# Optimization experiments

Measured on AMD Instinct MI355X. Metric: run time of the kernel, lower is better.

Reference implementation:

```python
import jax, jax.numpy as jnp
import numpy as np

B, LQ, LK = 8, 2048, 2048
HIST_DIM, COMB_DIM, FUSION_DIM = 1024, 1024, 1024


def _linear_params(key, in_dim, out_dim):
    k1, k2 = jax.random.split(key)
    bound = 1.0 / np.sqrt(in_dim)
    W = jax.random.uniform(k1, (out_dim, in_dim), jnp.float32, -bound, bound)
    b = jax.random.uniform(k2, (out_dim,), jnp.float32, -bound, bound)
    return W, b


def setup_inputs() -> dict:
    key = jax.random.key(0)
    ks = jax.random.split(key, 8)
    hW, hb = _linear_params(ks[0], HIST_DIM, FUSION_DIM)
    cW, cb = _linear_params(ks[1], COMB_DIM, FUSION_DIM)
    qW, qb = _linear_params(ks[2], FUSION_DIM, FUSION_DIM)
    kW, kb = _linear_params(ks[3], FUSION_DIM, FUSION_DIM)
    vW, vb = _linear_params(ks[4], FUSION_DIM, FUSION_DIM)
    oW, ob = _linear_params(ks[5], FUSION_DIM, FUSION_DIM)
    return {
        "history_features": jax.random.normal(ks[6], (B, LQ, HIST_DIM), jnp.float32),
        "combined_features": jax.random.normal(ks[7], (B, LK, COMB_DIM), jnp.float32),
        "hW": hW, "hb": hb, "cW": cW, "cb": cb,
        "qW": qW, "qb": qb, "kW": kW, "kb": kb,
        "vW": vW, "vb": vb, "oW": oW, "ob": ob,
    }


def _lin(x, W, b):
    # torch nn.Linear: y = x @ W.T + b
    return jnp.einsum('bld,fd->blf', x, W) + b


def reference(history_features, combined_features, hW, hb, cW, cb, qW, qb, kW, kb, vW, vb, oW, ob):
    h = _lin(history_features, hW, hb)      # [B, LQ, F]
    c = _lin(combined_features, cW, cb)     # [B, LK, F]
    q = _lin(h, qW, qb)
    k = _lin(c, kW, kb)
    v = _lin(c, vW, vb)
    scale = 1.0 / jnp.sqrt(jnp.float32(FUSION_DIM))
    scores = jnp.einsum('bqf,bkf->bqk', q, k) * scale
    attn = jax.nn.softmax(scores, axis=-1)
    attn_out = jnp.einsum('bqk,bkf->bqf', attn, v)
    return _lin(attn_out + q, oW, ob)
```

## Files before the change

### kernel.cpp

```cpp
#include <hip/hip_runtime.h>
#include <stdint.h>

using bf16x8 = __attribute__((ext_vector_type(8))) short;
using f32x4  = __attribute__((ext_vector_type(4))) float;
using u16x4  = __attribute__((ext_vector_type(4))) unsigned short;
using u16x8  = __attribute__((ext_vector_type(8))) unsigned short;

__device__ __forceinline__ unsigned short f2bf(float f) {
  unsigned u = __builtin_bit_cast(unsigned, f);
  u = (u + 0x7FFFu + ((u >> 16) & 1u)) >> 16;
  return (unsigned short)u;
}
__device__ __forceinline__ float bf2f(unsigned short h) {
  unsigned u = ((unsigned)h) << 16;
  return __builtin_bit_cast(float, u);
}

__global__ __launch_bounds__(256) void cvt_f32_to_bf16(
    const float* __restrict__ in, unsigned short* __restrict__ out, long n8) {
  long i = (long)blockIdx.x * blockDim.x + threadIdx.x;
  const long stride = (long)gridDim.x * blockDim.x;
  for (; i < n8; i += stride) {
    float4 a = ((const float4*)in)[2 * i];
    float4 b = ((const float4*)in)[2 * i + 1];
    u16x8 o = { f2bf(a.x), f2bf(a.y), f2bf(a.z), f2bf(a.w),
                f2bf(b.x), f2bf(b.y), f2bf(b.z), f2bf(b.w) };
    ((u16x8*)out)[i] = o;
  }
}

__global__ __launch_bounds__(256) void transpose_cast(
    const float* __restrict__ in, unsigned short* __restrict__ out, int R, int C) {
  __shared__ unsigned short tile[64][68];
  const int c0 = blockIdx.x * 64, r0 = blockIdx.y * 64;
  const int t = threadIdx.x;
#pragma unroll
  for (int i = 0; i < 4; ++i) {
    int ch = t + i * 256;
    int r = ch >> 4, c4 = (ch & 15) * 4;
    float4 v = *(const float4*)&in[(size_t)(r0 + r) * C + c0 + c4];
    u16x4 o = { f2bf(v.x), f2bf(v.y), f2bf(v.z), f2bf(v.w) };
    *(u16x4*)&tile[r][c4] = o;
  }
  __syncthreads();
#pragma unroll
  for (int i = 0; i < 4; ++i) {
    int ch = t + i * 256;
    int r = ch >> 4, c4 = (ch & 15) * 4;
    u16x4 v;
#pragma unroll
    for (int j = 0; j < 4; ++j) v[j] = tile[c4 + j][r];
    *(u16x4*)&out[(size_t)(c0 + r) * R + r0 + c4] = v;
  }
}

__global__ __launch_bounds__(256) void bias_matvec(
    const float* __restrict__ W, const float* __restrict__ x,
    const float* __restrict__ b, float* __restrict__ out, int n) {
  const int row = blockIdx.x;
  const float* wr = W + (long)row * n;
  float s = 0.f;
  for (int j = threadIdx.x; j < n; j += 256) s += wr[j] * x[j];
#pragma unroll
  for (int o = 32; o; o >>= 1) s += __shfl_xor(s, o);
  __shared__ float red[4];
  if ((threadIdx.x & 63) == 0) red[threadIdx.x >> 6] = s;
  __syncthreads();
  if (threadIdx.x == 0) out[row] = red[0] + red[1] + red[2] + red[3] + b[row];
}

__global__ __launch_bounds__(256) void merge_invl(
    const float* __restrict__ Lpart, float* __restrict__ invL, long nrows) {
  long r = (long)blockIdx.x * 256 + threadIdx.x;
  if (r < nrows) {
    const float* p = Lpart + r * 8;
    float s = 0.f;
#pragma unroll
    for (int i = 0; i < 8; ++i) s += p[i];
    invL[r] = 1.f / s;
  }
}

template <int EPI>
__global__ __launch_bounds__(256, 4) void gemm_bt(
    const unsigned short* __restrict__ A, const unsigned short* __restrict__ B,
    void* __restrict__ C, const float* __restrict__ bias,
    int M, int N, int K, float scale) {
  __shared__ unsigned short lA[2][128][32];
  __shared__ unsigned short lB[2][128][32];
  const int t = threadIdx.x;
  const int gx = gridDim.x, gy = gridDim.y;
  int bid = blockIdx.x + gx * blockIdx.y;
  const int nwg = gx * gy;
  const int chunk = nwg >> 3;
  int lid = (bid & 7) * chunk + (bid >> 3);
  const int bn = lid % gx;
  const int bm = lid / gx;

  const unsigned short* Ab = A + (long)bm * 128 * K;
  const unsigned short* Bb = B + (long)bn * 128 * K;

  const int lane = t & 63;
  const int wv = t >> 6, wm = wv >> 1, wn = wv & 1;
  const int fr = lane & 15, kg = lane >> 4;
  const int srow  = t >> 2;
  const int scol  = (t & 3) * 8;
  const int wbyte = (t >> 6) * 1024;

  f32x4 acc[4][4] = {};
  const int NT = K >> 5;

  auto stage = [&](int buf, int kt) {
    const unsigned short* sa = Ab + kt * 32;
    const unsigned short* sb = Bb + kt * 32;
#pragma unroll
    for (int p = 0; p < 2; ++p) {
      const unsigned short* srcA = sa + (long)(p * 64 + srow) * K + scol;
      const unsigned short* srcB = sb + (long)(p * 64 + srow) * K + scol;
      char* dA = (char*)(&lA[buf][0][0]) + p * 4096 + wbyte;
      char* dB = (char*)(&lB[buf][0][0]) + p * 4096 + wbyte;
      __builtin_amdgcn_global_load_lds(
          (const __attribute__((address_space(1))) void*)srcA,
          (__attribute__((address_space(3))) void*)dA, 16, 0, 0);
      __builtin_amdgcn_global_load_lds(
          (const __attribute__((address_space(1))) void*)srcB,
          (__attribute__((address_space(3))) void*)dB, 16, 0, 0);
    }
  };

  stage(0, 0);
  for (int kt = 0; kt < NT; ++kt) {
    const int cur = kt & 1;
    __syncthreads();
    if (kt + 1 < NT) stage(cur ^ 1, kt + 1);
    bf16x8 av[4], bv[4];
#pragma unroll
    for (int m = 0; m < 4; ++m)
      av[m] = *(const bf16x8*)&lA[cur][wm * 64 + m * 16 + fr][kg * 8];
#pragma unroll
    for (int n = 0; n < 4; ++n)
      bv[n] = *(const bf16x8*)&lB[cur][wn * 64 + n * 16 + fr][kg * 8];
#pragma unroll
    for (int m = 0; m < 4; ++m)
#pragma unroll
      for (int n = 0; n < 4; ++n)
        acc[m][n] = __builtin_amdgcn_mfma_f32_16x16x32_bf16(av[m], bv[n], acc[m][n], 0, 0, 0);
  }

  const int row0 = bm * 128 + wm * 64 + kg * 4;
  const int col0 = bn * 128 + wn * 64 + fr;
#pragma unroll
  for (int m = 0; m < 4; ++m)
#pragma unroll
    for (int n = 0; n < 4; ++n) {
      const int col = col0 + n * 16;
#pragma unroll
      for (int r = 0; r < 4; ++r) {
        const int row = row0 + m * 16 + r;
        float v = acc[m][n][r];
        if constexpr (EPI == 1) v *= scale; else v += bias[col];
        ((unsigned short*)C)[(long)row * N + col] = f2bf(v);
      }
    }
}

template <int EPI>
__global__ __launch_bounds__(512, 2) void gemm256(
    const unsigned short* __restrict__ A, const unsigned short* __restrict__ B,
    void* __restrict__ C, const float* __restrict__ bias,
    const unsigned short* __restrict__ resid, float* __restrict__ aux,
    int N, int K, long sA, long sB, long sC, long sR, float scale) {
  __shared__ char lds[131072];
  const int t = threadIdx.x;
  const int lane = t & 63, wid = t >> 6;

  const int gx = gridDim.x, gy = gridDim.y;
  int bid = blockIdx.x + gx * (blockIdx.y + gy * blockIdx.z);
  const int nwg = gx * gy * (int)gridDim.z;
  const int chunk = nwg >> 3;
  int lid = (bid & 7) * chunk + (bid >> 3);
  const int bn = lid % gx; lid /= gx;
  const int bm = lid % gy;
  const int bz = lid / gy;

  const unsigned short* Ab = A + (long)bz * sA + (long)bm * 256 * K;
  const unsigned short* Bb = B + (long)bz * sB + (long)bn * 256 * K;

  const int colswz = ((lane & 3) * 8) ^ ((lane >> 5) * 16);
  const int r0s = (wid >> 1) * 16 + (lane >> 2);
  const int scol = (wid & 1) * 32 + colswz;

  const int wm = wid >> 2, wn = wid & 3;
  const int fr = lane & 15, kg = lane >> 4;
  const int lanePart = (fr * 64 + kg * 16) ^ ((fr >> 3) << 5);

  auto issue = [&](const unsigned short* base, int kt, int h, int bufbyte) {
#pragma unroll
    for (int s = 0; s < 2; ++s) {
      const unsigned short* src = base + (long)(h * 128 + r0s + s * 64) * K + kt * 64 + scol;
      char* dst = lds + bufbyte + h * 16384 + s * 8192 + wid * 1024;
      __builtin_amdgcn_global_load_lds(
          (const __attribute__((address_space(1))) void*)src,
          (__attribute__((address_space(3))) void*)dst, 16, 0, 0);
    }
  };

  f32x4 acc[8][4] = {};
  const int NT = K >> 6;
  const int NITER = NT >> 1;

  issue(Ab, 0, 0, 0);      issue(Ab, 0, 1, 0);
  issue(Bb, 0, 0, 65536);  issue(Bb, 0, 1, 65536);
  issue(Bb, 1, 0, 98304);  issue(Bb, 1, 1, 98304);
  asm volatile("s_waitcnt vmcnt(4)" ::: "memory");
  __builtin_amdgcn_s_barrier();

  for (int it = 0; it < NITER; ++it) {
    const int kt0 = it * 2;
    const bool last = (it == NITER - 1);
#pragma unroll
    for (int hf = 0; hf < 2; ++hf) {
      const int abuf = hf * 32768;
      const int bbuf = 65536 + hf * 32768;
      bf16x8 bv[4][2];
      bf16x8 av[2][2];
#pragma unroll
      for (int mp = 0; mp < 4; ++mp) {
        if (mp == 0) {
#pragma unroll
          for (int n = 0; n < 4; ++n)
#pragma unroll
            for (int kk = 0; kk < 2; ++kk)
              bv[n][kk] = *(const bf16x8*)(lds + bbuf + ((wn * 4 + n) * 2 + kk) * 1024 + lanePart);
        }
#pragma unroll
        for (int ml = 0; ml < 2; ++ml)
#pragma unroll
          for (int kk = 0; kk < 2; ++kk)
            av[ml][kk] = *(const bf16x8*)(lds + abuf + ((wm * 8 + mp * 2 + ml) * 2 + kk) * 1024 + lanePart);
        if (hf == 0) {
          if (mp == 0) issue(Ab, kt0 + 1, 0, 32768);
          else if (mp == 1) { issue(Ab, kt0 + 1, 1, 32768); if (!last) issue(Bb, kt0 + 2, 0, 65536); }
          else if (mp == 2) { if (!last) issue(Bb, kt0 + 2, 1, 65536); }
          else {
            if (last) asm volatile("s_waitcnt vmcnt(0)" ::: "memory");
            else      asm volatile("s_waitcnt vmcnt(4)" ::: "memory");
          }
        } else if (!last) {
          if (mp == 0) issue(Ab, kt0 + 2, 0, 0);
          else if (mp == 1) { issue(Ab, kt0 + 2, 1, 0); issue(Bb, kt0 + 3, 0, 98304); }
          else if (mp == 2) issue(Bb, kt0 + 3, 1, 98304);
          else asm volatile("s_waitcnt vmcnt(4)" ::: "memory");
        }
        asm volatile("s_waitcnt lgkmcnt(0)" ::: "memory");
        __builtin_amdgcn_s_barrier();
        __builtin_amdgcn_s_setprio(1);
#pragma unroll
        for (int kk = 0; kk < 2; ++kk)
#pragma unroll
          for (int ml = 0; ml < 2; ++ml)
#pragma unroll
            for (int n = 0; n < 4; ++n)
              acc[mp * 2 + ml][n] = __builtin_amdgcn_mfma_f32_16x16x32_bf16(
                  av[ml][kk], bv[n][kk], acc[mp * 2 + ml][n], 0, 0, 0);
        __builtin_amdgcn_s_setprio(0);
      }
    }
  }

  const int row0 = bm * 256 + wm * 128 + kg * 4;
  const int col0 = bn * 256 + wn * 64 + fr;
  const long cb = (long)bz * sC;

  if constexpr (EPI == 5) {
    float* lf = (float*)lds;
#pragma unroll
    for (int m = 0; m < 8; ++m) {
#pragma unroll
      for (int r = 0; r < 4; ++r) {
        const int row = row0 + m * 16 + r;
        float sv = 0.f;
#pragma unroll
        for (int n = 0; n < 4; ++n) {
          float e = exp2f(acc[m][n][r] * scale);
          unsigned short eb = f2bf(e);
          ((unsigned short*)C)[cb + (long)row * N + col0 + n * 16] = eb;
          sv += bf2f(eb);
        }
#pragma unroll
        for (int o = 1; o < 16; o <<= 1) sv += __shfl_xor(sv, o);
        if ((lane & 15) == 0)
          lf[wn * 256 + wm * 128 + m * 16 + kg * 4 + r] = sv;
      }
    }
    __syncthreads();
    if (t < 256) {
      float s4 = lf[t] + lf[256 + t] + lf[512 + t] + lf[768 + t];
      aux[((long)bz * 2048 + bm * 256 + t) * 8 + bn] = s4;
    }
    return;
  }

#pragma unroll
  for (int m = 0; m < 8; ++m)
#pragma unroll
    for (int n = 0; n < 4; ++n) {
      const int col = col0 + n * 16;
#pragma unroll
      for (int r = 0; r < 4; ++r) {
        const int row = row0 + m * 16 + r;
        float v = acc[m][n][r];
        if constexpr (EPI == 0) {
          v += bias[col];
          ((unsigned short*)C)[cb + (long)row * N + col] = f2bf(v);
        } else if constexpr (EPI == 1) {
          v *= scale;
          ((unsigned short*)C)[cb + (long)row * N + col] = f2bf(v);
        } else if constexpr (EPI == 3) {
          v += bias[col];
          ((float*)C)[cb + (long)row * N + col] = v;
        } else if constexpr (EPI == 4) {
          v += bias[row];
          ((unsigned short*)C)[cb + (long)row * N + col] = f2bf(v);
        } else {
          v = v * bias[(long)bz * 2048 + row] + bf2f(resid[(long)bz * sR + (long)row * N + col]);
          ((unsigned short*)C)[cb + (long)row * N + col] = f2bf(v);
        }
      }
    }
}

extern "C" void kernel_launch(void* const* d_in, const int* in_sizes, int n_in,
                              void* d_out, int out_size, void* d_ws, size_t ws_size,
                              hipStream_t stream) {
  (void)in_sizes; (void)n_in; (void)out_size; (void)ws_size;
  const float* hist = (const float*)d_in[0];
  const float* comb = (const float*)d_in[1];
  const float* hW = (const float*)d_in[2];  const float* hb = (const float*)d_in[3];
  const float* cW = (const float*)d_in[4];  const float* cb = (const float*)d_in[5];
  const float* qW = (const float*)d_in[6];  const float* qb = (const float*)d_in[7];
  const float* kW = (const float*)d_in[8];
  const float* vW = (const float*)d_in[10]; const float* vb = (const float*)d_in[11];
  const float* oW = (const float*)d_in[12]; const float* ob = (const float*)d_in[13];

  constexpr int  Bn = 8, L = 2048, F = 1024;
  constexpr long NE = (long)Bn * L * F;
  constexpr long WE = (long)F * F;

  char* ws = (char*)d_ws;
  size_t off = 0;
  unsigned short* oWb = (unsigned short*)(ws + off); off += WE * 2;
  unsigned short* Wq  = (unsigned short*)(ws + off); off += WE * 2;
  unsigned short* Wkv = (unsigned short*)(ws + off); off += 2 * WE * 2;
  unsigned short* Wk  = Wkv;
  unsigned short* Wv  = Wkv + WE;
  float* bq = (float*)(ws + off); off += F * 4;
  float* bv = (float*)(ws + off); off += F * 4;
  float* Lpart = (float*)(ws + off); off += (size_t)Bn * L * 8 * 4;
  float* invL  = (float*)(ws + off); off += (size_t)Bn * L * 4;
  unsigned short* A0 = (unsigned short*)(ws + off); off += NE * 2;
  unsigned short* A1 = (unsigned short*)(ws + off); off += NE * 2;
  unsigned short* A2 = (unsigned short*)(ws + off); off += NE * 2;
  unsigned short* A3 = (unsigned short*)(ws + off); off += NE * 2;
  unsigned short* S  = (unsigned short*)(ws + off); off += (size_t)Bn * L * L * 2;
  unsigned short* hWt = S;
  unsigned short* cWt = S + WE;
  unsigned short* qWb = S + 2 * WE;
  unsigned short* kvWb = S + 3 * WE;

  transpose_cast<<<dim3(16, 16, 1), 256, 0, stream>>>(hW, hWt, F, F);
  transpose_cast<<<dim3(16, 16, 1), 256, 0, stream>>>(cW, cWt, F, F);
  cvt_f32_to_bf16<<<512, 256, 0, stream>>>(qW, qWb, WE / 8);
  cvt_f32_to_bf16<<<512, 256, 0, stream>>>(kW, kvWb, WE / 8);
  cvt_f32_to_bf16<<<512, 256, 0, stream>>>(vW, kvWb + WE, WE / 8);
  cvt_f32_to_bf16<<<512, 256, 0, stream>>>(oW, oWb, WE / 8);
  cvt_f32_to_bf16<<<2048, 256, 0, stream>>>(hist, A0, NE / 8);
  cvt_f32_to_bf16<<<2048, 256, 0, stream>>>(comb, A1, NE / 8);

  bias_matvec<<<F, 256, 0, stream>>>(qW, hb, qb, bq, F);
  bias_matvec<<<F, 256, 0, stream>>>(vW, cb, vb, bv, F);

  gemm_bt<1><<<dim3(8, 8, 1), 256, 0, stream>>>(qWb, hWt, Wq, nullptr,
      1024, 1024, 1024, 1.0f);
  gemm_bt<1><<<dim3(8, 16, 1), 256, 0, stream>>>(kvWb, cWt, Wkv, nullptr,
      2048, 1024, 1024, 1.0f);

  const float S2 = 0.03125f * 1.44269504089f;

  gemm256<0><<<dim3(4, 64, 1), 512, 0, stream>>>(A0, Wq, A2, bq, nullptr, nullptr,
      1024, 1024, 0, 0, 0, 0, 0.f);
  gemm256<1><<<dim3(4, 64, 1), 512, 0, stream>>>(A1, Wk, A0, nullptr, nullptr, nullptr,
      1024, 1024, 0, 0, 0, 0, 1.0f);
  gemm256<4><<<dim3(8, 4, Bn), 512, 0, stream>>>(Wv, A1, A3, bv, nullptr, nullptr,
      2048, 1024, 0, (long)L * F, (long)F * L, 0, 0.f);
  gemm256<5><<<dim3(8, 8, Bn), 512, 0, stream>>>(A2, A0, S, nullptr, nullptr, Lpart,
      2048, 1024, (long)L * F, (long)L * F, (long)L * L, 0, S2);
  merge_invl<<<64, 256, 0, stream>>>(Lpart, invL, (long)Bn * L);
  gemm256<6><<<dim3(4, 8, Bn), 512, 0, stream>>>(S, A3, A1, invL, A2, nullptr,
      1024, 2048, (long)L * L, (long)F * L, (long)L * F, (long)L * F, 0.f);
  gemm256<3><<<dim3(4, 64, 1), 512, 0, stream>>>(A1, oWb, (float*)d_out, ob, nullptr, nullptr,
      1024, 1024, 0, 0, 0, 0, 0.f);
}
```

Measured before the change: 393.9 us.

## Switch GEMM core to 32x32x16 MFMA with simple double-buffered K loop

Replaces the 16x16x32 MFMA tiling (acc[8][4]) with 32x32x16 MFMA (acc[4][2] of 16-wide vectors), changes the LDS read swizzle and fragment addressing to match, and rewrites the epilogues for the new accumulator layout. The fine-grained interleaved prefetch schedule with partial vmcnt waits is replaced by a plain per-tile double buffer that waits for all loads at the end of each K step. Larger MFMAs cut LDS fragment reads per flop, at the cost of less overlap between global loads and compute and one full barrier per tile.

```diff
diff --git a/kernel.cpp b/kernel.cpp
--- a/kernel.cpp
+++ b/kernel.cpp
@@ -3,6 +3,7 @@
 
 using bf16x8 = __attribute__((ext_vector_type(8))) short;
 using f32x4  = __attribute__((ext_vector_type(4))) float;
+using f32x16 = __attribute__((ext_vector_type(16))) float;
 using u16x4  = __attribute__((ext_vector_type(4))) unsigned short;
 using u16x8  = __attribute__((ext_vector_type(8))) unsigned short;
 
@@ -186,13 +187,9 @@
   const unsigned short* Ab = A + (long)bz * sA + (long)bm * 256 * K;
   const unsigned short* Bb = B + (long)bz * sB + (long)bn * 256 * K;
 
-  const int colswz = ((lane & 3) * 8) ^ ((lane >> 5) * 16);
+  const int colswz = (((lane & 3) * 8) ^ ((lane >> 5) * 16) ^ (((wid >> 1) & 1) << 3));
   const int r0s = (wid >> 1) * 16 + (lane >> 2);
   const int scol = (wid & 1) * 32 + colswz;
-
-  const int wm = wid >> 2, wn = wid & 3;
-  const int fr = lane & 15, kg = lane >> 4;
-  const int lanePart = (fr * 64 + kg * 16) ^ ((fr >> 3) << 5);
 
   auto issue = [&](const unsigned short* base, int kt, int h, int bufbyte) {
 #pragma unroll
@@ -204,93 +201,84 @@
           (__attribute__((address_space(3))) void*)dst, 16, 0, 0);
     }
   };
-
-  f32x4 acc[8][4] = {};
+  auto issueTile = [&](int kt, int buf) {
+    issue(Ab, kt, 0, buf * 32768);
+    issue(Ab, kt, 1, buf * 32768);
+    issue(Bb, kt, 0, 65536 + buf * 32768);
+    issue(Bb, kt, 1, 65536 + buf * 32768);
+  };
+
+  const int wm = wid >> 2, wn = wid & 3;
+  const int rl = lane & 31;
+  const int r15 = rl & 15, rsub = rl >> 4;
+  const int hi16b = (lane >> 5) * 16;
+  const int swzmask = ((r15 >> 3) << 5) ^ (rsub << 4);
+  const int laneBase = rsub * 2048 + r15 * 64;
+  int cp[4];
+#pragma unroll
+  for (int ks = 0; ks < 4; ++ks) {
+    const int cb = ks * 32 + hi16b;
+    cp[ks] = ((cb & 63) ^ swzmask) + ((cb >> 6) << 10);
+  }
+
+  f32x16 acc[4][2] = {};
   const int NT = K >> 6;
-  const int NITER = NT >> 1;
-
-  issue(Ab, 0, 0, 0);      issue(Ab, 0, 1, 0);
-  issue(Bb, 0, 0, 65536);  issue(Bb, 0, 1, 65536);
-  issue(Bb, 1, 0, 98304);  issue(Bb, 1, 1, 98304);
-  asm volatile("s_waitcnt vmcnt(4)" ::: "memory");
+
+  issueTile(0, 0);
+  asm volatile("s_waitcnt vmcnt(0)" ::: "memory");
   __builtin_amdgcn_s_barrier();
-
-  for (int it = 0; it < NITER; ++it) {
-    const int kt0 = it * 2;
-    const bool last = (it == NITER - 1);
-#pragma unroll
-    for (int hf = 0; hf < 2; ++hf) {
-      const int abuf = hf * 32768;
-      const int bbuf = 65536 + hf * 32768;
-      bf16x8 bv[4][2];
-      bf16x8 av[2][2];
-#pragma unroll
-      for (int mp = 0; mp < 4; ++mp) {
-        if (mp == 0) {
-#pragma unroll
-          for (int n = 0; n < 4; ++n)
-#pragma unroll
-            for (int kk = 0; kk < 2; ++kk)
-              bv[n][kk] = *(const bf16x8*)(lds + bbuf + ((wn * 4 + n) * 2 + kk) * 1024 + lanePart);
-        }
-#pragma unroll
-        for (int ml = 0; ml < 2; ++ml)
-#pragma unroll
-          for (int kk = 0; kk < 2; ++kk)
-            av[ml][kk] = *(const bf16x8*)(lds + abuf + ((wm * 8 + mp * 2 + ml) * 2 + kk) * 1024 + lanePart);
-        if (hf == 0) {
-          if (mp == 0) issue(Ab, kt0 + 1, 0, 32768);
-          else if (mp == 1) { issue(Ab, kt0 + 1, 1, 32768); if (!last) issue(Bb, kt0 + 2, 0, 65536); }
-          else if (mp == 2) { if (!last) issue(Bb, kt0 + 2, 1, 65536); }
-          else {
-            if (last) asm volatile("s_waitcnt vmcnt(0)" ::: "memory");
-            else      asm volatile("s_waitcnt vmcnt(4)" ::: "memory");
-          }
-        } else if (!last) {
-          if (mp == 0) issue(Ab, kt0 + 2, 0, 0);
-          else if (mp == 1) { issue(Ab, kt0 + 2, 1, 0); issue(Bb, kt0 + 3, 0, 98304); }
-          else if (mp == 2) issue(Bb, kt0 + 3, 1, 98304);
-          else asm volatile("s_waitcnt vmcnt(4)" ::: "memory");
-        }
-        asm volatile("s_waitcnt lgkmcnt(0)" ::: "memory");
-        __builtin_amdgcn_s_barrier();
-        __builtin_amdgcn_s_setprio(1);
-#pragma unroll
-        for (int kk = 0; kk < 2; ++kk)
-#pragma unroll
-          for (int ml = 0; ml < 2; ++ml)
-#pragma unroll
-            for (int n = 0; n < 4; ++n)
-              acc[mp * 2 + ml][n] = __builtin_amdgcn_mfma_f32_16x16x32_bf16(
-                  av[ml][kk], bv[n][kk], acc[mp * 2 + ml][n], 0, 0, 0);
-        __builtin_amdgcn_s_setprio(0);
+  asm volatile("" ::: "memory");
+
+  int cur = 0;
+  for (int kt = 0; kt < NT; ++kt) {
+    if (kt + 1 < NT) issueTile(kt + 1, cur ^ 1);
+    const char* ab = lds + cur * 32768;
+    const char* bb = lds + 65536 + cur * 32768;
+#pragma unroll
+    for (int ks = 0; ks < 4; ++ks) {
+      bf16x8 bf0 = *(const bf16x8*)(bb + (wn * 4 + 0) * 2048 + laneBase + cp[ks]);
+      bf16x8 bf1 = *(const bf16x8*)(bb + (wn * 4 + 2) * 2048 + laneBase + cp[ks]);
+      bf16x8 af[4];
+#pragma unroll
+      for (int mt = 0; mt < 4; ++mt)
+        af[mt] = *(const bf16x8*)(ab + (wm * 8 + mt * 2) * 2048 + laneBase + cp[ks]);
+#pragma unroll
+      for (int mt = 0; mt < 4; ++mt) {
+        acc[mt][0] = __builtin_amdgcn_mfma_f32_32x32x16_bf16(af[mt], bf0, acc[mt][0], 0, 0, 0);
+        acc[mt][1] = __builtin_amdgcn_mfma_f32_32x32x16_bf16(af[mt], bf1, acc[mt][1], 0, 0, 0);
       }
     }
-  }
-
-  const int row0 = bm * 256 + wm * 128 + kg * 4;
-  const int col0 = bn * 256 + wn * 64 + fr;
-  const long cb = (long)bz * sC;
+    asm volatile("s_waitcnt vmcnt(0) lgkmcnt(0)" ::: "memory");
+    __builtin_amdgcn_s_barrier();
+    asm volatile("" ::: "memory");
+    cur ^= 1;
+  }
+
+  const int cl = lane & 31;
+  const int rhalf = (lane >> 5) * 4;
+  const int row0g = bm * 256 + wm * 128;
+  const int col0g = bn * 256 + wn * 64;
+  const long cb2 = (long)bz * sC;
 
   if constexpr (EPI == 5) {
     float* lf = (float*)lds;
 #pragma unroll
-    for (int m = 0; m < 8; ++m) {
-#pragma unroll
-      for (int r = 0; r < 4; ++r) {
-        const int row = row0 + m * 16 + r;
+    for (int mt = 0; mt < 4; ++mt) {
+#pragma unroll
+      for (int reg = 0; reg < 16; ++reg) {
+        const int rit = (reg & 3) + ((reg >> 2) << 3) + rhalf;
+        const int row = row0g + mt * 32 + rit;
         float sv = 0.f;
 #pragma unroll
-        for (int n = 0; n < 4; ++n) {
-          float e = exp2f(acc[m][n][r] * scale);
+        for (int nt = 0; nt < 2; ++nt) {
+          float e = exp2f(acc[mt][nt][reg] * scale);
           unsigned short eb = f2bf(e);
-          ((unsigned short*)C)[cb + (long)row * N + col0 + n * 16] = eb;
+          ((unsigned short*)C)[cb2 + (long)row * N + col0g + nt * 32 + cl] = eb;
           sv += bf2f(eb);
         }
 #pragma unroll
-        for (int o = 1; o < 16; o <<= 1) sv += __shfl_xor(sv, o);
-        if ((lane & 15) == 0)
-          lf[wn * 256 + wm * 128 + m * 16 + kg * 4 + r] = sv;
+        for (int o = 1; o < 32; o <<= 1) sv += __shfl_xor(sv, o);
+        if (cl == 0) lf[wn * 256 + wm * 128 + mt * 32 + rit] = sv;
       }
     }
     __syncthreads();
@@ -302,29 +290,29 @@
   }
 
 #pragma unroll
-  for (int m = 0; m < 8; ++m)
-#pragma unroll
-    for (int n = 0; n < 4; ++n) {
-      const int col = col0 + n * 16;
-#pragma unroll
-      for (int r = 0; r < 4; ++r) {
-        const int row = row0 + m * 16 + r;
-        float v = acc[m][n][r];
+  for (int mt = 0; mt < 4; ++mt)
+#pragma unroll
+    for (int nt = 0; nt < 2; ++nt) {
+      const int col = col0g + nt * 32 + cl;
+#pragma unroll
+      for (int reg = 0; reg < 16; ++reg) {
+        const int row = row0g + mt * 32 + (reg & 3) + ((reg >> 2) << 3) + rhalf;
+        float v = acc[mt][nt][reg];
         if constexpr (EPI == 0) {
           v += bias[col];
-          ((unsigned short*)C)[cb + (long)row * N + col] = f2bf(v);
+          ((unsigned short*)C)[cb2 + (long)row * N + col] = f2bf(v);
         } else if constexpr (EPI == 1) {
           v *= scale;
-          ((unsigned short*)C)[cb + (long)row * N + col] = f2bf(v);
+          ((unsigned short*)C)[cb2 + (long)row * N + col] = f2bf(v);
         } else if constexpr (EPI == 3) {
           v += bias[col];
-          ((float*)C)[cb + (long)row * N + col] = v;
+          ((float*)C)[cb2 + (long)row * N + col] = v;
         } else if constexpr (EPI == 4) {
           v += bias[row];
-          ((unsigned short*)C)[cb + (long)row * N + col] = f2bf(v);
+          ((unsigned short*)C)[cb2 + (long)row * N + col] = f2bf(v);
         } else {
           v = v * bias[(long)bz * 2048 + row] + bf2f(resid[(long)bz * sR + (long)row * N + col]);
-          ((unsigned short*)C)[cb + (long)row * N + col] = f2bf(v);
+          ((unsigned short*)C)[cb2 + (long)row * N + col] = f2bf(v);
         }
       }
     }
```

Result: slower. 424.2 us (+7.7%).

## Replace 256x256 GEMM tiles with 128x128 double-buffered kernel

Applied to the files above, without the earlier changes.

Swaps the 512-thread 256x256-tile GEMM, with its finely interleaved load schedule, for a 256-thread 128x128-tile kernel using a simple double buffer and one barrier per k-step. Grids grow fourfold, and the row-sum partials for softmax normalisation double from 8 to 16 per row, so the merge kernel changes to match. The aim is more workgroups, better occupancy and a simpler pipeline. In exchange, operands are reused less per tile, more global and LDS traffic is needed, and the overlap of loads with MFMA work is coarser.

```diff
diff --git a/kernel.cpp b/kernel.cpp
--- a/kernel.cpp
+++ b/kernel.cpp
@@ -73,10 +73,10 @@
     const float* __restrict__ Lpart, float* __restrict__ invL, long nrows) {
   long r = (long)blockIdx.x * 256 + threadIdx.x;
   if (r < nrows) {
-    const float* p = Lpart + r * 8;
+    const float* p = Lpart + r * 16;
     float s = 0.f;
 #pragma unroll
-    for (int i = 0; i < 8; ++i) s += p[i];
+    for (int i = 0; i < 16; ++i) s += p[i];
     invL[r] = 1.f / s;
   }
 }
@@ -165,12 +165,12 @@
 }
 
 template <int EPI>
-__global__ __launch_bounds__(512, 2) void gemm256(
+__global__ __launch_bounds__(256, 2) void gemm128(
     const unsigned short* __restrict__ A, const unsigned short* __restrict__ B,
     void* __restrict__ C, const float* __restrict__ bias,
     const unsigned short* __restrict__ resid, float* __restrict__ aux,
     int N, int K, long sA, long sB, long sC, long sR, float scale) {
-  __shared__ char lds[131072];
+  __shared__ char lds[65536];
   const int t = threadIdx.x;
   const int lane = t & 63, wid = t >> 6;
 
@@ -183,99 +183,79 @@
   const int bm = lid % gy;
   const int bz = lid / gy;
 
-  const unsigned short* Ab = A + (long)bz * sA + (long)bm * 256 * K;
-  const unsigned short* Bb = B + (long)bz * sB + (long)bn * 256 * K;
+  const unsigned short* Ab = A + (long)bz * sA + (long)bm * 128 * K;
+  const unsigned short* Bb = B + (long)bz * sB + (long)bn * 128 * K;
 
   const int colswz = ((lane & 3) * 8) ^ ((lane >> 5) * 16);
   const int r0s = (wid >> 1) * 16 + (lane >> 2);
   const int scol = (wid & 1) * 32 + colswz;
-
-  const int wm = wid >> 2, wn = wid & 3;
+  const unsigned short* aCur = Ab + (long)r0s * K + scol;
+  const unsigned short* bCur = Bb + (long)r0s * K + scol;
+  const long offj = (long)32 * K;
+  const int dstB = wid * 1024;
+
+  auto stageTile = [&](const unsigned short* pa, const unsigned short* pb, int buf) {
+#pragma unroll
+    for (int j = 0; j < 4; ++j)
+      __builtin_amdgcn_global_load_lds(
+          (const __attribute__((address_space(1))) void*)(pa + j * offj),
+          (__attribute__((address_space(3))) void*)(lds + buf * 32768 + j * 4096 + dstB),
+          16, 0, 0);
+#pragma unroll
+    for (int j = 0; j < 4; ++j)
+      __builtin_amdgcn_global_load_lds(
+          (const __attribute__((address_space(1))) void*)(pb + j * offj),
+          (__attribute__((address_space(3))) void*)(lds + buf * 32768 + 16384 + j * 4096 + dstB),
+          16, 0, 0);
+  };
+
+  const int wm = wid >> 1, wn = wid & 1;
   const int fr = lane & 15, kg = lane >> 4;
-  const int lanePart = (fr * 64 + kg * 16) ^ ((fr >> 3) << 5);
-
-  auto issue = [&](const unsigned short* base, int kt, int h, int bufbyte) {
-#pragma unroll
-    for (int s = 0; s < 2; ++s) {
-      const unsigned short* src = base + (long)(h * 128 + r0s + s * 64) * K + kt * 64 + scol;
-      char* dst = lds + bufbyte + h * 16384 + s * 8192 + wid * 1024;
-      __builtin_amdgcn_global_load_lds(
-          (const __attribute__((address_space(1))) void*)src,
-          (__attribute__((address_space(3))) void*)dst, 16, 0, 0);
-    }
-  };
-
-  f32x4 acc[8][4] = {};
+  const int lanePart = fr * 64 + ((kg * 16) ^ ((fr >> 3) << 5));
+
+  f32x4 acc[4][4] = {};
   const int NT = K >> 6;
-  const int NITER = NT >> 1;
-
-  issue(Ab, 0, 0, 0);      issue(Ab, 0, 1, 0);
-  issue(Bb, 0, 0, 65536);  issue(Bb, 0, 1, 65536);
-  issue(Bb, 1, 0, 98304);  issue(Bb, 1, 1, 98304);
-  asm volatile("s_waitcnt vmcnt(4)" ::: "memory");
+
+  stageTile(aCur, bCur, 0);
+  aCur += 64; bCur += 64;
+  asm volatile("s_waitcnt vmcnt(0)" ::: "memory");
   __builtin_amdgcn_s_barrier();
 
-  for (int it = 0; it < NITER; ++it) {
-    const int kt0 = it * 2;
-    const bool last = (it == NITER - 1);
-#pragma unroll
-    for (int hf = 0; hf < 2; ++hf) {
-      const int abuf = hf * 32768;
-      const int bbuf = 65536 + hf * 32768;
-      bf16x8 bv[4][2];
-      bf16x8 av[2][2];
-#pragma unroll
-      for (int mp = 0; mp < 4; ++mp) {
-        if (mp == 0) {
-#pragma unroll
-          for (int n = 0; n < 4; ++n)
-#pragma unroll
-            for (int kk = 0; kk < 2; ++kk)
-              bv[n][kk] = *(const bf16x8*)(lds + bbuf + ((wn * 4 + n) * 2 + kk) * 1024 + lanePart);
-        }
-#pragma unroll
-        for (int ml = 0; ml < 2; ++ml)
-#pragma unroll
-          for (int kk = 0; kk < 2; ++kk)
-            av[ml][kk] = *(const bf16x8*)(lds + abuf + ((wm * 8 + mp * 2 + ml) * 2 + kk) * 1024 + lanePart);
-        if (hf == 0) {
-          if (mp == 0) issue(Ab, kt0 + 1, 0, 32768);
-          else if (mp == 1) { issue(Ab, kt0 + 1, 1, 32768); if (!last) issue(Bb, kt0 + 2, 0, 65536); }
-          else if (mp == 2) { if (!last) issue(Bb, kt0 + 2, 1, 65536); }
-          else {
-            if (last) asm volatile("s_waitcnt vmcnt(0)" ::: "memory");
-            else      asm volatile("s_waitcnt vmcnt(4)" ::: "memory");
-          }
-        } else if (!last) {
-          if (mp == 0) issue(Ab, kt0 + 2, 0, 0);
-          else if (mp == 1) { issue(Ab, kt0 + 2, 1, 0); issue(Bb, kt0 + 3, 0, 98304); }
-          else if (mp == 2) issue(Bb, kt0 + 3, 1, 98304);
-          else asm volatile("s_waitcnt vmcnt(4)" ::: "memory");
-        }
-        asm volatile("s_waitcnt lgkmcnt(0)" ::: "memory");
-        __builtin_amdgcn_s_barrier();
-        __builtin_amdgcn_s_setprio(1);
-#pragma unroll
-        for (int kk = 0; kk < 2; ++kk)
-#pragma unroll
-          for (int ml = 0; ml < 2; ++ml)
-#pragma unroll
-            for (int n = 0; n < 4; ++n)
-              acc[mp * 2 + ml][n] = __builtin_amdgcn_mfma_f32_16x16x32_bf16(
-                  av[ml][kk], bv[n][kk], acc[mp * 2 + ml][n], 0, 0, 0);
-        __builtin_amdgcn_s_setprio(0);
+  for (int kt = 0; kt < NT; ++kt) {
+    const int buf = kt & 1;
+    if (kt + 1 < NT) { stageTile(aCur, bCur, buf ^ 1); aCur += 64; bCur += 64; }
+    const char* aB = lds + buf * 32768 + wm * 8192 + lanePart;
+    const char* bB = lds + buf * 32768 + 16384 + wn * 8192 + lanePart;
+    bf16x8 av[4][2], bv[4][2];
+#pragma unroll
+    for (int m = 0; m < 4; ++m)
+#pragma unroll
+      for (int kk = 0; kk < 2; ++kk) {
+        av[m][kk] = *(const bf16x8*)(aB + m * 2048 + kk * 1024);
+        bv[m][kk] = *(const bf16x8*)(bB + m * 2048 + kk * 1024);
       }
-    }
-  }
-
-  const int row0 = bm * 256 + wm * 128 + kg * 4;
-  const int col0 = bn * 256 + wn * 64 + fr;
+    __builtin_amdgcn_s_setprio(1);
+#pragma unroll
+    for (int kk = 0; kk < 2; ++kk)
+#pragma unroll
+      for (int m = 0; m < 4; ++m)
+#pragma unroll
+        for (int n = 0; n < 4; ++n)
+          acc[m][n] = __builtin_amdgcn_mfma_f32_16x16x32_bf16(
+              av[m][kk], bv[n][kk], acc[m][n], 0, 0, 0);
+    __builtin_amdgcn_s_setprio(0);
+    asm volatile("s_waitcnt vmcnt(0) lgkmcnt(0)" ::: "memory");
+    __builtin_amdgcn_s_barrier();
+  }
+
+  const int row0 = bm * 128 + wm * 64 + kg * 4;
+  const int col0 = bn * 128 + wn * 64 + fr;
   const long cb = (long)bz * sC;
 
   if constexpr (EPI == 5) {
     float* lf = (float*)lds;
 #pragma unroll
-    for (int m = 0; m < 8; ++m) {
+    for (int m = 0; m < 4; ++m) {
 #pragma unroll
       for (int r = 0; r < 4; ++r) {
         const int row = row0 + m * 16 + r;
@@ -290,19 +270,19 @@
 #pragma unroll
         for (int o = 1; o < 16; o <<= 1) sv += __shfl_xor(sv, o);
         if ((lane & 15) == 0)
-          lf[wn * 256 + wm * 128 + m * 16 + kg * 4 + r] = sv;
+          lf[wn * 128 + wm * 64 + m * 16 + kg * 4 + r] = sv;
       }
     }
     __syncthreads();
-    if (t < 256) {
-      float s4 = lf[t] + lf[256 + t] + lf[512 + t] + lf[768 + t];
-      aux[((long)bz * 2048 + bm * 256 + t) * 8 + bn] = s4;
+    if (t < 128) {
+      float s2 = lf[t] + lf[128 + t];
+      aux[((long)bz * 2048 + bm * 128 + t) * 16 + bn] = s2;
     }
     return;
   }
 
 #pragma unroll
-  for (int m = 0; m < 8; ++m)
+  for (int m = 0; m < 4; ++m)
 #pragma unroll
     for (int n = 0; n < 4; ++n) {
       const int col = col0 + n * 16;
@@ -356,7 +336,7 @@
   unsigned short* Wv  = Wkv + WE;
   float* bq = (float*)(ws + off); off += F * 4;
   float* bv = (float*)(ws + off); off += F * 4;
-  float* Lpart = (float*)(ws + off); off += (size_t)Bn * L * 8 * 4;
+  float* Lpart = (float*)(ws + off); off += (size_t)Bn * L * 16 * 4;
   float* invL  = (float*)(ws + off); off += (size_t)Bn * L * 4;
   unsigned short* A0 = (unsigned short*)(ws + off); off += NE * 2;
   unsigned short* A1 = (unsigned short*)(ws + off); off += NE * 2;
@@ -387,17 +367,17 @@
 
   const float S2 = 0.03125f * 1.44269504089f;
 
-  gemm256<0><<<dim3(4, 64, 1), 512, 0, stream>>>(A0, Wq, A2, bq, nullptr, nullptr,
+  gemm128<0><<<dim3(8, 128, 1), 256, 0, stream>>>(A0, Wq, A2, bq, nullptr, nullptr,
       1024, 1024, 0, 0, 0, 0, 0.f);
-  gemm256<1><<<dim3(4, 64, 1), 512, 0, stream>>>(A1, Wk, A0, nullptr, nullptr, nullptr,
+  gemm128<1><<<dim3(8, 128, 1), 256, 0, stream>>>(A1, Wk, A0, nullptr, nullptr, nullptr,
       1024, 1024, 0, 0, 0, 0, 1.0f);
-  gemm256<4><<<dim3(8, 4, Bn), 512, 0, stream>>>(Wv, A1, A3, bv, nullptr, nullptr,
+  gemm128<4><<<dim3(16, 8, Bn), 256, 0, stream>>>(Wv, A1, A3, bv, nullptr, nullptr,
       2048, 1024, 0, (long)L * F, (long)F * L, 0, 0.f);
-  gemm256<5><<<dim3(8, 8, Bn), 512, 0, stream>>>(A2, A0, S, nullptr, nullptr, Lpart,
+  gemm128<5><<<dim3(16, 16, Bn), 256, 0, stream>>>(A2, A0, S, nullptr, nullptr, Lpart,
       2048, 1024, (long)L * F, (long)L * F, (long)L * L, 0, S2);
   merge_invl<<<64, 256, 0, stream>>>(Lpart, invL, (long)Bn * L);
-  gemm256<6><<<dim3(4, 8, Bn), 512, 0, stream>>>(S, A3, A1, invL, A2, nullptr,
+  gemm128<6><<<dim3(8, 16, Bn), 256, 0, stream>>>(S, A3, A1, invL, A2, nullptr,
       1024, 2048, (long)L * L, (long)F * L, (long)L * F, (long)L * F, 0.f);
-  gemm256<3><<<dim3(4, 64, 1), 512, 0, stream>>>(A1, oWb, (float*)d_out, ob, nullptr, nullptr,
+  gemm128<3><<<dim3(8, 128, 1), 256, 0, stream>>>(A1, oWb, (float*)d_out, ob, nullptr, nullptr,
       1024, 1024, 0, 0, 0, 0, 0.f);
 }
```

Measured after the change: 418.7 us. 6.3% more time.
